# Kernel tuning notes

Hardware: AMD Instinct MI355X
Metric: run time of the kernel (lower is better)

The kernel has to match this reference:

```python
import jax, jax.numpy as jnp
import numpy as np

B = 100000          # graphs per batch
NPG = 9             # nodes per graph (2 stations + 7)
N = B * NPG         # total nodes
EPG = 36            # edges per graph
E = B * EPG         # total edges
F_IN, H1, H2 = 16, 32, 64
STATION_NODE_IDS = (0, 8)


def setup_inputs() -> dict:
    key = jax.random.key(0)
    ks = jax.random.split(key, 12)
    x = jax.random.normal(ks[0], (N, F_IN), dtype=jnp.float32)
    # random intra-graph edges, then offset by 9*graph_id so edges never cross graphs
    src_local = jax.random.randint(ks[1], (E,), 0, NPG)
    dst_local = jax.random.randint(ks[2], (E,), 0, NPG)
    offsets = jnp.repeat(jnp.arange(B, dtype=jnp.int32) * NPG, EPG)
    edge_index = jnp.stack([src_local + offsets, dst_local + offsets]).astype(jnp.int32)
    batch = (jnp.arange(N, dtype=jnp.int32) // NPG)

    def lin(k, fan_in, fan_out):
        s = 1.0 / np.sqrt(fan_in)
        kw, kb = jax.random.split(k)
        W = jax.random.uniform(kw, (fan_in, fan_out), jnp.float32, -s, s)
        b = jax.random.uniform(kb, (fan_out,), jnp.float32, -s, s)
        return W, b

    W1, b1 = lin(ks[3], F_IN, H1)
    W2, b2 = lin(ks[4], H1, H2)
    fc1_w, fc1_b = lin(ks[5], H2 + H2, 64)
    fc2_w, fc2_b = lin(ks[6], 64, 1)
    return {"x": x, "edge_index": edge_index, "batch": batch,
            "W1": W1, "b1": b1, "W2": W2, "b2": b2,
            "fc1_w": fc1_w, "fc1_b": fc1_b, "fc2_w": fc2_w, "fc2_b": fc2_b}


def gcn_conv(x, W, b, src, dst):
    """PyG GCNConv: add self-loops, symmetric D^-1/2 (A+I) D^-1/2 normalization."""
    n = x.shape[0]
    h = x @ W                                  # [N, out]
    loop = jnp.arange(n, dtype=src.dtype)
    src_sl = jnp.concatenate([src, loop])
    dst_sl = jnp.concatenate([dst, loop])
    deg = jax.ops.segment_sum(jnp.ones(src_sl.shape[0], h.dtype), dst_sl, num_segments=n)
    dinv = jnp.where(deg > 0, jax.lax.rsqrt(deg), 0.0)
    norm = dinv[src_sl] * dinv[dst_sl]         # [E+N]
    out = jax.ops.segment_sum(norm[:, None] * h[src_sl], dst_sl, num_segments=n)
    return out + b


def reference(x, edge_index, batch, W1, b1, W2, b2, fc1_w, fc1_b, fc2_w, fc2_b):
    src, dst = edge_index[0], edge_index[1]
    h = jax.nn.relu(gcn_conv(x, W1, b1, src, dst))
    h = jax.nn.relu(gcn_conv(h, W2, b2, src, dst))
    num_graphs = h.shape[0] // NPG
    counts = jax.ops.segment_sum(jnp.ones(h.shape[0], h.dtype), batch, num_segments=num_graphs)
    global_ctx = jax.ops.segment_sum(h, batch, num_segments=num_graphs) / counts[:, None]
    qs = []
    base = jnp.arange(num_graphs) * NPG
    for node_id in STATION_NODE_IDS:
        station_emb = h[base + node_id]                         # [B, 64]
        combined = jnp.concatenate([station_emb, global_ctx], axis=1)  # [B, 128]
        q = jax.nn.relu(combined @ fc1_w + fc1_b) @ fc2_w + fc2_b      # [B, 1]
        qs.append(q)
    return jnp.concatenate(qs, axis=1)                          # [B, 2]
```

## Files before the change

kernel.cpp:

```cpp
#include <hip/hip_runtime.h>

#define NGRAPH 100000
#define NPG 9
#define EPG 36

#define WPB 8
#define BLOCK (WPB * 64)
#define GRID 1024

#define WSYNC() asm volatile("s_waitcnt lgkmcnt(0)" ::: "memory")

__device__ __forceinline__ float rl(float v, int l) {
  return __uint_as_float(__builtin_amdgcn_readlane(__float_as_uint(v), l));
}

struct __align__(16) WS {
  float xg[144];
  float A[108];
  float deg[12];
  float h1[288];
};

__global__ __launch_bounds__(BLOCK, 2) void gqn(
    const float* __restrict__ x,
    const int* __restrict__ ei,
    const float* __restrict__ W1, const float* __restrict__ b1,
    const float* __restrict__ W2, const float* __restrict__ b2,
    const float* __restrict__ fc1w, const float* __restrict__ fc1b,
    const float* __restrict__ fc2w, const float* __restrict__ fc2b,
    float* __restrict__ out)
{
  __shared__ float fc1T[64 * 132];
  __shared__ WS ws[WPB];

  const int tid  = threadIdx.x;
  const int lane = tid & 63;
  const int wib  = tid >> 6;

  for (int idx = tid; idx < 128 * 64; idx += BLOCK) {
    int k = idx >> 6, j = idx & 63;
    fc1T[j * 132 + k] = fc1w[idx];
  }
  __syncthreads();

  const int f1 = lane & 31;
  float w1c[16], w2c[32];
#pragma unroll
  for (int k = 0; k < 16; ++k) w1c[k] = W1[k * 32 + f1];
  const float b1c = b1[f1];
#pragma unroll
  for (int k = 0; k < 32; ++k) w2c[k] = W2[k * 64 + lane];
  const float b2c   = b2[lane];
  const float fc1bc = fc1b[lane];
  const float fc2wc = fc2w[lane];
  const float fc2bs = fc2b[0];

  WS* S = &ws[wib];
  const int* srcp = ei;
  const int* dstp = ei + NGRAPH * EPG;
  const int gw = blockIdx.x * WPB + wib;
  const int nw = GRID * WPB;

  for (int g = gw; g < NGRAPH; g += nw) {
    WSYNC();

    if (lane < 36) {
      float4 v = ((const float4*)(x + (long)g * 144))[lane];
      ((float4*)S->xg)[lane] = v;
    }
    if (lane < 27) ((float4*)S->A)[lane] = make_float4(0.f, 0.f, 0.f, 0.f);
    if (lane < 9)  S->deg[lane] = 1.0f;
    int es = 0, ed = 0;
    if (lane < 36) {
      es = srcp[g * EPG + lane] - g * NPG;
      ed = dstp[g * EPG + lane] - g * NPG;
    }
    WSYNC();

    if (lane < 36) atomicAdd(&S->deg[ed], 1.0f);
    WSYNC();

    if (lane < 9) S->deg[lane] = 1.0f / sqrtf(S->deg[lane]);
    WSYNC();

    if (lane < 36) {
      float nv = S->deg[es] * S->deg[ed];
      atomicAdd(&S->A[ed * 12 + es], nv);
    }
    if (lane < 9) {
      float dv = S->deg[lane];
      atomicAdd(&S->A[lane * 12 + lane], dv * dv);
    }

    float h1t[9];
#pragma unroll
    for (int n = 0; n < 9; ++n) {
      float acc = 0.f;
#pragma unroll
      for (int q = 0; q < 4; ++q) {
        float4 xv = ((const float4*)S->xg)[n * 4 + q];
        acc = fmaf(xv.x, w1c[q * 4 + 0], acc);
        acc = fmaf(xv.y, w1c[q * 4 + 1], acc);
        acc = fmaf(xv.z, w1c[q * 4 + 2], acc);
        acc = fmaf(xv.w, w1c[q * 4 + 3], acc);
      }
      h1t[n] = acc;
    }
    WSYNC();

#pragma unroll
    for (int n = 0; n < 9; ++n) {
      const float4* Ar = (const float4*)(S->A + n * 12);
      float4 a0 = Ar[0], a1 = Ar[1];
      float  a8 = S->A[n * 12 + 8];
      float acc = b1c;
      acc = fmaf(a0.x, h1t[0], acc);
      acc = fmaf(a0.y, h1t[1], acc);
      acc = fmaf(a0.z, h1t[2], acc);
      acc = fmaf(a0.w, h1t[3], acc);
      acc = fmaf(a1.x, h1t[4], acc);
      acc = fmaf(a1.y, h1t[5], acc);
      acc = fmaf(a1.z, h1t[6], acc);
      acc = fmaf(a1.w, h1t[7], acc);
      acc = fmaf(a8,   h1t[8], acc);
      if (lane < 32) S->h1[n * 32 + f1] = fmaxf(acc, 0.f);
    }
    WSYNC();

    float h2t[9];
#pragma unroll
    for (int n = 0; n < 9; ++n) {
      float acc = 0.f;
#pragma unroll
      for (int q = 0; q < 8; ++q) {
        float4 hv = ((const float4*)S->h1)[n * 8 + q];
        acc = fmaf(hv.x, w2c[q * 4 + 0], acc);
        acc = fmaf(hv.y, w2c[q * 4 + 1], acc);
        acc = fmaf(hv.z, w2c[q * 4 + 2], acc);
        acc = fmaf(hv.w, w2c[q * 4 + 3], acc);
      }
      h2t[n] = acc;
    }

    float e0 = 0.f, e8 = 0.f, ctx = 0.f;
#pragma unroll
    for (int n = 0; n < 9; ++n) {
      const float4* Ar = (const float4*)(S->A + n * 12);
      float4 a0 = Ar[0], a1 = Ar[1];
      float  a8 = S->A[n * 12 + 8];
      float acc = b2c;
      acc = fmaf(a0.x, h2t[0], acc);
      acc = fmaf(a0.y, h2t[1], acc);
      acc = fmaf(a0.z, h2t[2], acc);
      acc = fmaf(a0.w, h2t[3], acc);
      acc = fmaf(a1.x, h2t[4], acc);
      acc = fmaf(a1.y, h2t[5], acc);
      acc = fmaf(a1.z, h2t[6], acc);
      acc = fmaf(a1.w, h2t[7], acc);
      acc = fmaf(a8,   h2t[8], acc);
      float r = fmaxf(acc, 0.f);
      ctx += r;
      if (n == 0) e0 = r;
      if (n == 8) e8 = r;
    }
    ctx *= (1.f / 9.f);

    float acc0 = fc1bc, acc8 = fc1bc, accC = 0.f;
    const float4* Wrow = (const float4*)(fc1T + lane * 132);
#pragma unroll
    for (int q = 0; q < 16; ++q) {
      float4 wv = Wrow[q];
      acc0 = fmaf(wv.x, rl(e0, 4 * q + 0), acc0);
      acc0 = fmaf(wv.y, rl(e0, 4 * q + 1), acc0);
      acc0 = fmaf(wv.z, rl(e0, 4 * q + 2), acc0);
      acc0 = fmaf(wv.w, rl(e0, 4 * q + 3), acc0);
      acc8 = fmaf(wv.x, rl(e8, 4 * q + 0), acc8);
      acc8 = fmaf(wv.y, rl(e8, 4 * q + 1), acc8);
      acc8 = fmaf(wv.z, rl(e8, 4 * q + 2), acc8);
      acc8 = fmaf(wv.w, rl(e8, 4 * q + 3), acc8);
    }
#pragma unroll
    for (int q = 16; q < 32; ++q) {
      float4 wv = Wrow[q];
      int kb = 4 * (q - 16);
      accC = fmaf(wv.x, rl(ctx, kb + 0), accC);
      accC = fmaf(wv.y, rl(ctx, kb + 1), accC);
      accC = fmaf(wv.z, rl(ctx, kb + 2), accC);
      accC = fmaf(wv.w, rl(ctx, kb + 3), accC);
    }
    float r0 = fmaxf(acc0 + accC, 0.f);
    float r8 = fmaxf(acc8 + accC, 0.f);

    float p0 = r0 * fc2wc;
    float p8 = r8 * fc2wc;
#pragma unroll
    for (int off = 32; off; off >>= 1) {
      p0 += __shfl_xor(p0, off);
      p8 += __shfl_xor(p8, off);
    }
    if (lane == 0) {
      out[2 * g + 0] = p0 + fc2bs;
      out[2 * g + 1] = p8 + fc2bs;
    }
  }
}

extern "C" void kernel_launch(void* const* d_in, const int* in_sizes, int n_in,
                              void* d_out, int out_size, void* d_ws, size_t ws_size,
                              hipStream_t stream) {
  const float* x    = (const float*)d_in[0];
  const int*   ei   = (const int*)d_in[1];
  const float* W1   = (const float*)d_in[3];
  const float* b1   = (const float*)d_in[4];
  const float* W2   = (const float*)d_in[5];
  const float* b2   = (const float*)d_in[6];
  const float* fc1w = (const float*)d_in[7];
  const float* fc1b = (const float*)d_in[8];
  const float* fc2w = (const float*)d_in[9];
  const float* fc2b = (const float*)d_in[10];
  float* out = (float*)d_out;

  hipLaunchKernelGGL(gqn, dim3(GRID), dim3(BLOCK), 0, stream,
                     x, ei, W1, b1, W2, b2, fc1w, fc1b, fc2w, fc2b, out);
}
```

Before: 449.7 us.

## Prefetch next graph, compute degrees via ballot, use packed FMA, move fc1 transpose to global

Several changes land at once. Each graph's x and edge indices are now loaded into registers one iteration ahead. Node degrees are counted with wavefront ballots and popcount, and dinv is gathered with ds_bpermute, which removes the shared-memory degree array and its atomic/sync rounds. The dense GCN math uses packed v2f FMAs. The fc1 weight transpose moves from per-block LDS setup into a separate small kernel writing a global buffer, and blocks shrink to 4 waves with an occupancy hint of 4. In exchange, fc1 weights are now read from global/cache on every graph instead of LDS, and a second launch is added.

```diff
diff --git a/kernel.cpp b/kernel.cpp
--- a/kernel.cpp
+++ b/kernel.cpp
@@ -3,53 +3,59 @@
 #define NGRAPH 100000
 #define NPG 9
 #define EPG 36
-
-#define WPB 8
+#define WPB 4
 #define BLOCK (WPB * 64)
 #define GRID 1024
 
+typedef float v2f __attribute__((ext_vector_type(2)));
+
 #define WSYNC() asm volatile("s_waitcnt lgkmcnt(0)" ::: "memory")
 
 __device__ __forceinline__ float rl(float v, int l) {
   return __uint_as_float(__builtin_amdgcn_readlane(__float_as_uint(v), l));
+}
+__device__ __forceinline__ v2f pkfma(v2f a, v2f b, v2f c) {
+  return __builtin_elementwise_fma(a, b, c);
+}
+
+__device__ float g_fc1T[64 * 128];
+
+__global__ void tr_kernel(const float* __restrict__ w) {
+  int t = blockIdx.x * 256 + threadIdx.x;
+  int k = t >> 6, j = t & 63;
+  g_fc1T[j * 128 + k] = w[t];
 }
 
 struct __align__(16) WS {
   float xg[144];
   float A[108];
-  float deg[12];
   float h1[288];
 };
 
-__global__ __launch_bounds__(BLOCK, 2) void gqn(
+__global__ __launch_bounds__(BLOCK, 4) void gqn(
     const float* __restrict__ x,
     const int* __restrict__ ei,
     const float* __restrict__ W1, const float* __restrict__ b1,
     const float* __restrict__ W2, const float* __restrict__ b2,
-    const float* __restrict__ fc1w, const float* __restrict__ fc1b,
+    const float* __restrict__ fc1b,
     const float* __restrict__ fc2w, const float* __restrict__ fc2b,
     float* __restrict__ out)
 {
-  __shared__ float fc1T[64 * 132];
   __shared__ WS ws[WPB];
 
   const int tid  = threadIdx.x;
   const int lane = tid & 63;
   const int wib  = tid >> 6;
-
-  for (int idx = tid; idx < 128 * 64; idx += BLOCK) {
-    int k = idx >> 6, j = idx & 63;
-    fc1T[j * 132 + k] = fc1w[idx];
-  }
-  __syncthreads();
-
-  const int f1 = lane & 31;
-  float w1c[16], w2c[32];
-#pragma unroll
-  for (int k = 0; k < 16; ++k) w1c[k] = W1[k * 32 + f1];
+  const int f1   = lane & 31;
+
+  v2f w1p[8], w2p[16];
+#pragma unroll
+  for (int q = 0; q < 8; ++q)
+    w1p[q] = (v2f){W1[(2*q+0)*32 + f1], W1[(2*q+1)*32 + f1]};
   const float b1c = b1[f1];
 #pragma unroll
-  for (int k = 0; k < 32; ++k) w2c[k] = W2[k * 64 + lane];
+  for (int q = 0; q < 16; ++q)
+    w2p[q] = (v2f){W2[(2*q+0)*64 + lane], W2[(2*q+1)*64 + lane]};
   const float b2c   = b2[lane];
   const float fc1bc = fc1b[lane];
   const float fc2wc = fc2w[lane];
@@ -61,132 +67,138 @@
   const int gw = blockIdx.x * WPB + wib;
   const int nw = GRID * WPB;
 
+  float4 xv = make_float4(0.f, 0.f, 0.f, 0.f);
+  int es = -1, ed = -1;
+  if (gw < NGRAPH && lane < 36) {
+    xv = ((const float4*)(x + (size_t)gw * 144))[lane];
+    es = srcp[gw * EPG + lane] - gw * NPG;
+    ed = dstp[gw * EPG + lane] - gw * NPG;
+  }
+
   for (int g = gw; g < NGRAPH; g += nw) {
+    if (lane < 36) ((float4*)S->xg)[lane] = xv;
+    if (lane < 27) ((float4*)S->A)[lane] = make_float4(0.f, 0.f, 0.f, 0.f);
+
+    float4 xv2 = make_float4(0.f, 0.f, 0.f, 0.f);
+    int es2 = -1, ed2 = -1;
+    const int g2 = g + nw;
+    if (g2 < NGRAPH && lane < 36) {
+      xv2 = ((const float4*)(x + (size_t)g2 * 144))[lane];
+      es2 = srcp[g2 * EPG + lane] - g2 * NPG;
+      ed2 = dstp[g2 * EPG + lane] - g2 * NPG;
+    }
+
+    int cnt = 0;
+#pragma unroll
+    for (int n = 0; n < 9; ++n) {
+      unsigned long long bm = __ballot(ed == n);
+      if (lane == n) cnt = (int)__popcll(bm);
+    }
+    float dvl = 0.f;
+    if (lane < 9) dvl = rsqrtf(1.f + (float)cnt);
+
+    float dv_s = __int_as_float(__builtin_amdgcn_ds_bpermute(es << 2, __float_as_int(dvl)));
+    float dv_d = __int_as_float(__builtin_amdgcn_ds_bpermute(ed << 2, __float_as_int(dvl)));
+    float nrm = dv_s * dv_d;
+
+    if (lane < 36) atomicAdd(&S->A[ed * 12 + es], nrm);
+    if (lane < 9)  atomicAdd(&S->A[lane * 12 + lane], dvl * dvl);
+
+    float h1t[9];
+#pragma unroll
+    for (int n = 0; n < 9; ++n) {
+      const float4* xr = (const float4*)(S->xg + n * 16);
+      float4 x0 = xr[0], x1 = xr[1], x2 = xr[2], x3 = xr[3];
+      v2f acc = (v2f){0.f, 0.f};
+      acc = pkfma((v2f){x0.x, x0.y}, w1p[0], acc);
+      acc = pkfma((v2f){x0.z, x0.w}, w1p[1], acc);
+      acc = pkfma((v2f){x1.x, x1.y}, w1p[2], acc);
+      acc = pkfma((v2f){x1.z, x1.w}, w1p[3], acc);
+      acc = pkfma((v2f){x2.x, x2.y}, w1p[4], acc);
+      acc = pkfma((v2f){x2.z, x2.w}, w1p[5], acc);
+      acc = pkfma((v2f){x3.x, x3.y}, w1p[6], acc);
+      acc = pkfma((v2f){x3.z, x3.w}, w1p[7], acc);
+      h1t[n] = acc.x + acc.y;
+    }
     WSYNC();
 
-    if (lane < 36) {
-      float4 v = ((const float4*)(x + (long)g * 144))[lane];
-      ((float4*)S->xg)[lane] = v;
-    }
-    if (lane < 27) ((float4*)S->A)[lane] = make_float4(0.f, 0.f, 0.f, 0.f);
-    if (lane < 9)  S->deg[lane] = 1.0f;
-    int es = 0, ed = 0;
-    if (lane < 36) {
-      es = srcp[g * EPG + lane] - g * NPG;
-      ed = dstp[g * EPG + lane] - g * NPG;
+    {
+      v2f hp0 = (v2f){h1t[0], h1t[1]}, hp1 = (v2f){h1t[2], h1t[3]};
+      v2f hp2 = (v2f){h1t[4], h1t[5]}, hp3 = (v2f){h1t[6], h1t[7]};
+#pragma unroll
+      for (int n = 0; n < 9; ++n) {
+        const float4* Ar = (const float4*)(S->A + n * 12);
+        float4 a0 = Ar[0], a1 = Ar[1];
+        float  a8 = S->A[n * 12 + 8];
+        v2f acc = (v2f){0.f, 0.f};
+        acc = pkfma((v2f){a0.x, a0.y}, hp0, acc);
+        acc = pkfma((v2f){a0.z, a0.w}, hp1, acc);
+        acc = pkfma((v2f){a1.x, a1.y}, hp2, acc);
+        acc = pkfma((v2f){a1.z, a1.w}, hp3, acc);
+        float r = fmaf(a8, h1t[8], acc.x + acc.y + b1c);
+        if (lane < 32) S->h1[n * 32 + f1] = fmaxf(r, 0.f);
+      }
     }
     WSYNC();
 
-    if (lane < 36) atomicAdd(&S->deg[ed], 1.0f);
-    WSYNC();
-
-    if (lane < 9) S->deg[lane] = 1.0f / sqrtf(S->deg[lane]);
-    WSYNC();
-
-    if (lane < 36) {
-      float nv = S->deg[es] * S->deg[ed];
-      atomicAdd(&S->A[ed * 12 + es], nv);
-    }
-    if (lane < 9) {
-      float dv = S->deg[lane];
-      atomicAdd(&S->A[lane * 12 + lane], dv * dv);
-    }
-
-    float h1t[9];
+    float h2t[9];
 #pragma unroll
     for (int n = 0; n < 9; ++n) {
-      float acc = 0.f;
-#pragma unroll
-      for (int q = 0; q < 4; ++q) {
-        float4 xv = ((const float4*)S->xg)[n * 4 + q];
-        acc = fmaf(xv.x, w1c[q * 4 + 0], acc);
-        acc = fmaf(xv.y, w1c[q * 4 + 1], acc);
-        acc = fmaf(xv.z, w1c[q * 4 + 2], acc);
-        acc = fmaf(xv.w, w1c[q * 4 + 3], acc);
+      const float4* hr = (const float4*)(S->h1 + n * 32);
+      v2f acc = (v2f){0.f, 0.f};
+#pragma unroll
+      for (int q = 0; q < 8; ++q) {
+        float4 hv = hr[q];
+        acc = pkfma((v2f){hv.x, hv.y}, w2p[2*q+0], acc);
+        acc = pkfma((v2f){hv.z, hv.w}, w2p[2*q+1], acc);
       }
-      h1t[n] = acc;
-    }
-    WSYNC();
-
-#pragma unroll
-    for (int n = 0; n < 9; ++n) {
-      const float4* Ar = (const float4*)(S->A + n * 12);
-      float4 a0 = Ar[0], a1 = Ar[1];
-      float  a8 = S->A[n * 12 + 8];
-      float acc = b1c;
-      acc = fmaf(a0.x, h1t[0], acc);
-      acc = fmaf(a0.y, h1t[1], acc);
-      acc = fmaf(a0.z, h1t[2], acc);
-      acc = fmaf(a0.w, h1t[3], acc);
-      acc = fmaf(a1.x, h1t[4], acc);
-      acc = fmaf(a1.y, h1t[5], acc);
-      acc = fmaf(a1.z, h1t[6], acc);
-      acc = fmaf(a1.w, h1t[7], acc);
-      acc = fmaf(a8,   h1t[8], acc);
-      if (lane < 32) S->h1[n * 32 + f1] = fmaxf(acc, 0.f);
-    }
-    WSYNC();
-
-    float h2t[9];
-#pragma unroll
-    for (int n = 0; n < 9; ++n) {
-      float acc = 0.f;
-#pragma unroll
-      for (int q = 0; q < 8; ++q) {
-        float4 hv = ((const float4*)S->h1)[n * 8 + q];
-        acc = fmaf(hv.x, w2c[q * 4 + 0], acc);
-        acc = fmaf(hv.y, w2c[q * 4 + 1], acc);
-        acc = fmaf(hv.z, w2c[q * 4 + 2], acc);
-        acc = fmaf(hv.w, w2c[q * 4 + 3], acc);
+      h2t[n] = acc.x + acc.y;
+    }
+
+    float e0 = 0.f, e8 = 0.f, ctx = 0.f;
+    {
+      v2f gp0 = (v2f){h2t[0], h2t[1]}, gp1 = (v2f){h2t[2], h2t[3]};
+      v2f gp2 = (v2f){h2t[4], h2t[5]}, gp3 = (v2f){h2t[6], h2t[7]};
+#pragma unroll
+      for (int n = 0; n < 9; ++n) {
+        const float4* Ar = (const float4*)(S->A + n * 12);
+        float4 a0 = Ar[0], a1 = Ar[1];
+        float  a8 = S->A[n * 12 + 8];
+        v2f acc = (v2f){0.f, 0.f};
+        acc = pkfma((v2f){a0.x, a0.y}, gp0, acc);
+        acc = pkfma((v2f){a0.z, a0.w}, gp1, acc);
+        acc = pkfma((v2f){a1.x, a1.y}, gp2, acc);
+        acc = pkfma((v2f){a1.z, a1.w}, gp3, acc);
+        float r = fmaxf(fmaf(a8, h2t[8], acc.x + acc.y + b2c), 0.f);
+        ctx += r;
+        if (n == 0) e0 = r;
+        if (n == 8) e8 = r;
       }
-      h2t[n] = acc;
-    }
-
-    float e0 = 0.f, e8 = 0.f, ctx = 0.f;
-#pragma unroll
-    for (int n = 0; n < 9; ++n) {
-      const float4* Ar = (const float4*)(S->A + n * 12);
-      float4 a0 = Ar[0], a1 = Ar[1];
-      float  a8 = S->A[n * 12 + 8];
-      float acc = b2c;
-      acc = fmaf(a0.x, h2t[0], acc);
-      acc = fmaf(a0.y, h2t[1], acc);
-      acc = fmaf(a0.z, h2t[2], acc);
-      acc = fmaf(a0.w, h2t[3], acc);
-      acc = fmaf(a1.x, h2t[4], acc);
-      acc = fmaf(a1.y, h2t[5], acc);
-      acc = fmaf(a1.z, h2t[6], acc);
-      acc = fmaf(a1.w, h2t[7], acc);
-      acc = fmaf(a8,   h2t[8], acc);
-      float r = fmaxf(acc, 0.f);
-      ctx += r;
-      if (n == 0) e0 = r;
-      if (n == 8) e8 = r;
     }
     ctx *= (1.f / 9.f);
 
     float acc0 = fc1bc, acc8 = fc1bc, accC = 0.f;
-    const float4* Wrow = (const float4*)(fc1T + lane * 132);
+    const float4* Wrow = (const float4*)(g_fc1T + lane * 128);
 #pragma unroll
     for (int q = 0; q < 16; ++q) {
       float4 wv = Wrow[q];
-      acc0 = fmaf(wv.x, rl(e0, 4 * q + 0), acc0);
-      acc0 = fmaf(wv.y, rl(e0, 4 * q + 1), acc0);
-      acc0 = fmaf(wv.z, rl(e0, 4 * q + 2), acc0);
-      acc0 = fmaf(wv.w, rl(e0, 4 * q + 3), acc0);
-      acc8 = fmaf(wv.x, rl(e8, 4 * q + 0), acc8);
-      acc8 = fmaf(wv.y, rl(e8, 4 * q + 1), acc8);
-      acc8 = fmaf(wv.z, rl(e8, 4 * q + 2), acc8);
-      acc8 = fmaf(wv.w, rl(e8, 4 * q + 3), acc8);
+      acc0 = fmaf(wv.x, rl(e0, 4*q+0), acc0);
+      acc0 = fmaf(wv.y, rl(e0, 4*q+1), acc0);
+      acc0 = fmaf(wv.z, rl(e0, 4*q+2), acc0);
+      acc0 = fmaf(wv.w, rl(e0, 4*q+3), acc0);
+      acc8 = fmaf(wv.x, rl(e8, 4*q+0), acc8);
+      acc8 = fmaf(wv.y, rl(e8, 4*q+1), acc8);
+      acc8 = fmaf(wv.z, rl(e8, 4*q+2), acc8);
+      acc8 = fmaf(wv.w, rl(e8, 4*q+3), acc8);
     }
 #pragma unroll
     for (int q = 16; q < 32; ++q) {
       float4 wv = Wrow[q];
       int kb = 4 * (q - 16);
-      accC = fmaf(wv.x, rl(ctx, kb + 0), accC);
-      accC = fmaf(wv.y, rl(ctx, kb + 1), accC);
-      accC = fmaf(wv.z, rl(ctx, kb + 2), accC);
-      accC = fmaf(wv.w, rl(ctx, kb + 3), accC);
+      accC = fmaf(wv.x, rl(ctx, kb+0), accC);
+      accC = fmaf(wv.y, rl(ctx, kb+1), accC);
+      accC = fmaf(wv.z, rl(ctx, kb+2), accC);
+      accC = fmaf(wv.w, rl(ctx, kb+3), accC);
     }
     float r0 = fmaxf(acc0 + accC, 0.f);
     float r8 = fmaxf(acc8 + accC, 0.f);
@@ -199,9 +211,10 @@
       p8 += __shfl_xor(p8, off);
     }
     if (lane == 0) {
-      out[2 * g + 0] = p0 + fc2bs;
-      out[2 * g + 1] = p8 + fc2bs;
-    }
+      ((float2*)out)[g] = make_float2(p0 + fc2bs, p8 + fc2bs);
+    }
+
+    xv = xv2; es = es2; ed = ed2;
   }
 }
 
@@ -220,6 +233,7 @@
   const float* fc2b = (const float*)d_in[10];
   float* out = (float*)d_out;
 
+  hipLaunchKernelGGL(tr_kernel, dim3(32), dim3(256), 0, stream, fc1w);
   hipLaunchKernelGGL(gqn, dim3(GRID), dim3(BLOCK), 0, stream,
-                     x, ei, W1, b1, W2, b2, fc1w, fc1b, fc2w, fc2b, out);
-}
+                     x, ei, W1, b1, W2, b2, fc1b, fc2w, fc2b, out);
+}
```

New measurement: 1.027 ms. 2.28x slower.
